# Kernel optimization log

Hardware: AMD Instinct MI355X
Metric: run time of the kernel (lower is better)

Reference implementation:

```python
import jax, jax.numpy as jnp
import numpy as np

EPS = 1e-9
SPREAD_WEIGHT = 0.1
QUAD_WEIGHT = 1.0

N_NODES = 200000
N_EDGES = 12800000
DIM = 128


def to_uhg_space(x):
    # dim > 2: truncate to first 2 features, append homogeneous 1 -> [..., 3]
    ones = jnp.ones((*x.shape[:-1], 1), dtype=x.dtype)
    return jnp.concatenate([x[..., :2], ones], axis=-1)


def uhg_inner(a, b):
    # -<spatial,spatial> + time*time, keepdim
    return -jnp.sum(a[..., :-1] * b[..., :-1], axis=-1, keepdims=True) + a[..., -1:] * b[..., -1:]


def uhg_quadrance(a, b):
    aa = uhg_inner(a, a)
    bb = uhg_inner(b, b)
    ab = uhg_inner(a, b)
    num = ab * ab - aa * bb
    den = aa * bb
    safe = jnp.maximum(jnp.abs(den), EPS) * jnp.sign(den)
    return (num / safe).squeeze(-1)


# spread has the identical formula, applied to lines instead of points
uhg_spread = uhg_quadrance


def setup_inputs() -> dict:
    key = jax.random.key(0)
    k1, k2 = jax.random.split(key)
    z = jax.random.normal(k1, (N_NODES, DIM), dtype=jnp.float32)
    edge_index = jax.random.randint(k2, (2, N_EDGES), 0, N_NODES, dtype=jnp.int32)
    return {"z": z, "edge_index": edge_index}


def reference(z, edge_index):
    z_uhg = to_uhg_space(z)                      # [N, 3]
    src, dst = edge_index[0], edge_index[1]
    # proximity: quadrance over all edges (gather + fused elementwise + mean)
    quad = uhg_quadrance(z_uhg[src], z_uhg[dst])  # [E]
    proximity_loss = quad.mean()
    # compactness: quadrance of every node to the origin [0,0,1]
    origin = jnp.zeros((1, 3), dtype=z.dtype).at[:, -1].set(1.0)
    compactness_loss = uhg_quadrance(z_uhg, origin).mean()
    # lines: vectorized cross product of each point with the origin
    lines = jnp.cross(z_uhg, origin)              # [N, 3]
    # spread over the first min(10, E) edges only (as in the original)
    n_sp = min(10, edge_index.shape[1])
    sp = uhg_spread(lines[src[:n_sp]], lines[dst[:n_sp]])
    spread_loss = sp.mean()
    loss = QUAD_WEIGHT * (proximity_loss + compactness_loss) + SPREAD_WEIGHT * spread_loss
    return loss
```

## Files before the change

kernel.cpp:

```cpp
#include <hip/hip_runtime.h>
#include <hip/hip_bf16.h>

#define UHG_EPS 1e-9
#define ZDIM 128

#define EDGE_BLOCKS 2048
#define NODE_BLOCKS 1024
#define BLOCK 256

#define PROX_OFF 0
#define COMP_OFF (16 * 1024)
#define TABLE_OFF (24 * 1024)

typedef float vfloat2 __attribute__((ext_vector_type(2)));
typedef int vint4 __attribute__((ext_vector_type(4)));

__device__ vfloat2 llvm_amdgcn_raw_buffer_load_v2f32(vint4 rsrc, int voffset, int soffset,
                                                     int cpol) __asm("llvm.amdgcn.raw.buffer.load.v2f32");

__device__ __forceinline__ vint4 make_srd(const void* base, unsigned int bytes) {
    union { const void* p; unsigned int w[2]; } pb;
    pb.p = base;
    vint4 r;
    r.x = (int)pb.w[0];
    r.y = (int)pb.w[1];
    r.z = (int)bytes;
    r.w = 0x00020000;
    return r;
}


__device__ __forceinline__ double safe_den(double den) {
    return copysign(fmax(fabs(den), UHG_EPS), den);
}

__device__ __forceinline__ double quad_xy(vfloat2 a, vfloat2 b) {
    double xa = a.x, ya = a.y, xb = b.x, yb = b.y;
    double aa = 1.0 - (xa * xa + ya * ya);
    double bb = 1.0 - (xb * xb + yb * yb);
    double ab = 1.0 - (xa * xb + ya * yb);
    double den = aa * bb;
    double num = ab * ab - den;
    return num / safe_den(den);
}

__device__ __forceinline__ double block_reduce(double v, double* sh) {
    int lane = threadIdx.x & 63;
    int wid = threadIdx.x >> 6;
    v += __shfl_down(v, 32);
    v += __shfl_down(v, 16);
    v += __shfl_down(v, 8);
    v += __shfl_down(v, 4);
    v += __shfl_down(v, 2);
    v += __shfl_down(v, 1);
    if (lane == 0) sh[wid] = v;
    __syncthreads();
    double r = 0.0;
    if (wid == 0) {
        int nw = blockDim.x >> 6;
        r = (lane < nw) ? sh[lane] : 0.0;
        r += __shfl_down(r, 4);
        r += __shfl_down(r, 2);
        r += __shfl_down(r, 1);
    }
    __syncthreads();
    return r;
}


__global__ __launch_bounds__(BLOCK) void node_kernel(const float* __restrict__ z,
                                                     vfloat2* __restrict__ table,
                                                     double* __restrict__ comp_partials, int N) {
    __shared__ double sh[8];
    const vfloat2* zp = (const vfloat2*)z;
    double local = 0.0;
    for (int i = blockIdx.x * BLOCK + threadIdx.x; i < N; i += NODE_BLOCKS * BLOCK) {
        vfloat2 v = zp[(size_t)i * (ZDIM / 2)];
        if (table) table[i] = v;
        double x = v.x, y = v.y;
        double aa = 1.0 - (x * x + y * y);
        local += (1.0 - aa) / safe_den(aa);
    }
    double tot = block_reduce(local, sh);
    if (threadIdx.x == 0) comp_partials[blockIdx.x] = tot;
}

template <int COMPACT>
__global__ __launch_bounds__(BLOCK) void edge_kernel(const vint4* __restrict__ src4,
                                                     const vint4* __restrict__ dst4, int nvec,
                                                     const int* __restrict__ src,
                                                     const int* __restrict__ dst, int E,
                                                     const void* __restrict__ xy, int N,
                                                     double* __restrict__ prox_partials) {
    __shared__ double sh[8];
    double local = 0.0;
    int tid = blockIdx.x * BLOCK + threadIdx.x;
    const int gstride = EDGE_BLOCKS * BLOCK;
    const int SHIFT = COMPACT ? 3 : 9;

    vint4 srd = make_srd(xy, COMPACT ? (unsigned int)N * 8u : (unsigned int)N * 512u);

    int nvec2 = nvec / 2;
    int v = tid;
    vint4 s0n = {}, s1n = {}, d0n = {}, d1n = {};
    if (v < nvec2) {
        s0n = __builtin_nontemporal_load(src4 + 2 * v);
        s1n = __builtin_nontemporal_load(src4 + 2 * v + 1);
        d0n = __builtin_nontemporal_load(dst4 + 2 * v);
        d1n = __builtin_nontemporal_load(dst4 + 2 * v + 1);
    }
    while (v < nvec2) {
        vint4 s0 = s0n, s1 = s1n, d0 = d0n, d1 = d1n;
        int vn = v + gstride;
        if (vn < nvec2) {
            s0n = __builtin_nontemporal_load(src4 + 2 * vn);
            s1n = __builtin_nontemporal_load(src4 + 2 * vn + 1);
            d0n = __builtin_nontemporal_load(dst4 + 2 * vn);
            d1n = __builtin_nontemporal_load(dst4 + 2 * vn + 1);
        }
        vfloat2 a0 = llvm_amdgcn_raw_buffer_load_v2f32(srd, s0.x << SHIFT, 0, 1);
        vfloat2 a1 = llvm_amdgcn_raw_buffer_load_v2f32(srd, s0.y << SHIFT, 0, 1);
        vfloat2 a2 = llvm_amdgcn_raw_buffer_load_v2f32(srd, s0.z << SHIFT, 0, 1);
        vfloat2 a3 = llvm_amdgcn_raw_buffer_load_v2f32(srd, s0.w << SHIFT, 0, 1);
        vfloat2 a4 = llvm_amdgcn_raw_buffer_load_v2f32(srd, s1.x << SHIFT, 0, 1);
        vfloat2 a5 = llvm_amdgcn_raw_buffer_load_v2f32(srd, s1.y << SHIFT, 0, 1);
        vfloat2 a6 = llvm_amdgcn_raw_buffer_load_v2f32(srd, s1.z << SHIFT, 0, 1);
        vfloat2 a7 = llvm_amdgcn_raw_buffer_load_v2f32(srd, s1.w << SHIFT, 0, 1);
        vfloat2 b0 = llvm_amdgcn_raw_buffer_load_v2f32(srd, d0.x << SHIFT, 0, 1);
        vfloat2 b1 = llvm_amdgcn_raw_buffer_load_v2f32(srd, d0.y << SHIFT, 0, 1);
        vfloat2 b2 = llvm_amdgcn_raw_buffer_load_v2f32(srd, d0.z << SHIFT, 0, 1);
        vfloat2 b3 = llvm_amdgcn_raw_buffer_load_v2f32(srd, d0.w << SHIFT, 0, 1);
        vfloat2 b4 = llvm_amdgcn_raw_buffer_load_v2f32(srd, d1.x << SHIFT, 0, 1);
        vfloat2 b5 = llvm_amdgcn_raw_buffer_load_v2f32(srd, d1.y << SHIFT, 0, 1);
        vfloat2 b6 = llvm_amdgcn_raw_buffer_load_v2f32(srd, d1.z << SHIFT, 0, 1);
        vfloat2 b7 = llvm_amdgcn_raw_buffer_load_v2f32(srd, d1.w << SHIFT, 0, 1);
        local += quad_xy(a0, b0);
        local += quad_xy(a1, b1);
        local += quad_xy(a2, b2);
        local += quad_xy(a3, b3);
        local += quad_xy(a4, b4);
        local += quad_xy(a5, b5);
        local += quad_xy(a6, b6);
        local += quad_xy(a7, b7);
        v = vn;
    }
    for (int e = 8 * nvec2 + tid; e < E; e += gstride) {
        vfloat2 a = llvm_amdgcn_raw_buffer_load_v2f32(srd, src[e] << SHIFT, 0, 1);
        vfloat2 b = llvm_amdgcn_raw_buffer_load_v2f32(srd, dst[e] << SHIFT, 0, 1);
        local += quad_xy(a, b);
    }
    double tot = block_reduce(local, sh);
    if (threadIdx.x == 0) prox_partials[blockIdx.x] = tot;
}

__global__ __launch_bounds__(BLOCK) void finalize_kernel(const int* __restrict__ src,
                                                         const int* __restrict__ dst,
                                                         const float* __restrict__ z,
                                                         const double* __restrict__ prox_partials,
                                                         const double* __restrict__ comp_partials,
                                                         float* __restrict__ out, int N, int E) {
    __shared__ double sh[8];
    int t = threadIdx.x;

    double pl = 0.0;
    for (int i = t; i < EDGE_BLOCKS; i += BLOCK) pl += prox_partials[i];
    double prox = block_reduce(pl, sh);

    double cl = 0.0;
    for (int i = t; i < NODE_BLOCKS; i += BLOCK) cl += comp_partials[i];
    double comp = block_reduce(cl, sh);

    int n_sp = E < 10 ? E : 10;
    double sl = 0.0;
    if (t < n_sp) {
        int s = src[t], d = dst[t];
        double xa = z[(size_t)s * ZDIM], ya = z[(size_t)s * ZDIM + 1];
        double xb = z[(size_t)d * ZDIM], yb = z[(size_t)d * ZDIM + 1];
        double aa = -(ya * ya + xa * xa);
        double bb = -(yb * yb + xb * xb);
        double ab = -(ya * yb + xa * xb);
        double den = aa * bb;
        sl = (ab * ab - den) / safe_den(den);
    }
    double spread = block_reduce(sl, sh);

    if (t == 0) {
        double loss = prox / (double)E + comp / (double)N;
        if (n_sp > 0) loss += 0.1 * (spread / (double)n_sp);
        out[0] = (float)loss;
    }
}


extern "C" void kernel_launch(void* const* d_in, const int* in_sizes, int n_in,
                              void* d_out, int out_size, void* d_ws, size_t ws_size,
                              hipStream_t stream) {
    const float* z = (const float*)d_in[0];
    const int* edge_index = (const int*)d_in[1];
    float* out = (float*)d_out;

    const int N = in_sizes[0] / ZDIM;
    const int E = in_sizes[1] / 2;
    const int* src = edge_index;
    const int* dst = edge_index + (size_t)E;

    double* prox_partials = (double*)((char*)d_ws + PROX_OFF);
    double* comp_partials = (double*)((char*)d_ws + COMP_OFF);
    vfloat2* table = (vfloat2*)((char*)d_ws + TABLE_OFF);
    bool use_table = ws_size >= TABLE_OFF + (size_t)N * sizeof(vfloat2);

    node_kernel<<<NODE_BLOCKS, BLOCK, 0, stream>>>(z, use_table ? table : nullptr,
                                                   comp_partials, N);

    int nvec = E / 4;
    if (use_table) {
        edge_kernel<1><<<EDGE_BLOCKS, BLOCK, 0, stream>>>((const vint4*)src, (const vint4*)dst,
                                                          nvec, src, dst, E, table, N,
                                                          prox_partials);
    } else {
        edge_kernel<0><<<EDGE_BLOCKS, BLOCK, 0, stream>>>((const vint4*)src, (const vint4*)dst,
                                                          nvec, src, dst, E, z, N,
                                                          prox_partials);
    }

    finalize_kernel<<<1, BLOCK, 0, stream>>>(src, dst, z, prox_partials, comp_partials,
                                             out, N, E);
}
```

Baseline: 294.1 us.

## Software-pipeline edge gathers two iterations deep and halve edge grid

Restructures the edge loop into a two-stage software pipeline. Each iteration issues the table gathers for the next batch of 8 edges and loads the index vectors two batches ahead, then does the quadrance math on the current batch. A sched_barrier keeps the compiler from reordering the loads past the compute. The edge grid also drops from 2048 to 1024 blocks, so each thread covers more iterations and the pipeline has more steady-state work. The cost is higher register pressure from the 32 extra in-flight float2 values, which may lower occupancy.

```diff
diff --git a/kernel.cpp b/kernel.cpp
--- a/kernel.cpp
+++ b/kernel.cpp
@@ -4,7 +4,7 @@
 #define UHG_EPS 1e-9
 #define ZDIM 128
 
-#define EDGE_BLOCKS 2048
+#define EDGE_BLOCKS 1024
 #define NODE_BLOCKS 1024
 #define BLOCK 256
 
@@ -85,6 +85,16 @@
     if (threadIdx.x == 0) comp_partials[blockIdx.x] = tot;
 }
 
+#define GATHER8(dsta, i0, i1)                                                   \
+    dsta[0] = llvm_amdgcn_raw_buffer_load_v2f32(srd, (i0).x << SHIFT, 0, 1);    \
+    dsta[1] = llvm_amdgcn_raw_buffer_load_v2f32(srd, (i0).y << SHIFT, 0, 1);    \
+    dsta[2] = llvm_amdgcn_raw_buffer_load_v2f32(srd, (i0).z << SHIFT, 0, 1);    \
+    dsta[3] = llvm_amdgcn_raw_buffer_load_v2f32(srd, (i0).w << SHIFT, 0, 1);    \
+    dsta[4] = llvm_amdgcn_raw_buffer_load_v2f32(srd, (i1).x << SHIFT, 0, 1);    \
+    dsta[5] = llvm_amdgcn_raw_buffer_load_v2f32(srd, (i1).y << SHIFT, 0, 1);    \
+    dsta[6] = llvm_amdgcn_raw_buffer_load_v2f32(srd, (i1).z << SHIFT, 0, 1);    \
+    dsta[7] = llvm_amdgcn_raw_buffer_load_v2f32(srd, (i1).w << SHIFT, 0, 1);
+
 template <int COMPACT>
 __global__ __launch_bounds__(BLOCK) void edge_kernel(const vint4* __restrict__ src4,
                                                      const vint4* __restrict__ dst4, int nvec,
@@ -101,49 +111,54 @@
     vint4 srd = make_srd(xy, COMPACT ? (unsigned int)N * 8u : (unsigned int)N * 512u);
 
     int nvec2 = nvec / 2;
-    int v = tid;
-    vint4 s0n = {}, s1n = {}, d0n = {}, d1n = {};
-    if (v < nvec2) {
-        s0n = __builtin_nontemporal_load(src4 + 2 * v);
-        s1n = __builtin_nontemporal_load(src4 + 2 * v + 1);
-        d0n = __builtin_nontemporal_load(dst4 + 2 * v);
-        d1n = __builtin_nontemporal_load(dst4 + 2 * v + 1);
-    }
-    while (v < nvec2) {
-        vint4 s0 = s0n, s1 = s1n, d0 = d0n, d1 = d1n;
-        int vn = v + gstride;
-        if (vn < nvec2) {
-            s0n = __builtin_nontemporal_load(src4 + 2 * vn);
-            s1n = __builtin_nontemporal_load(src4 + 2 * vn + 1);
-            d0n = __builtin_nontemporal_load(dst4 + 2 * vn);
-            d1n = __builtin_nontemporal_load(dst4 + 2 * vn + 1);
+
+    int v0 = tid;
+    bool p0 = v0 < nvec2;
+    int v1 = v0 + gstride;
+    bool p1 = v1 < nvec2;
+
+    vint4 is0 = {}, is1 = {}, id0 = {}, id1 = {};
+    vfloat2 ca[8] = {}, cb[8] = {};
+    vfloat2 na[8] = {}, nb[8] = {};
+
+    if (p0) {
+        vint4 s0 = __builtin_nontemporal_load(src4 + 2 * (long)v0);
+        vint4 s1 = __builtin_nontemporal_load(src4 + 2 * (long)v0 + 1);
+        vint4 d0 = __builtin_nontemporal_load(dst4 + 2 * (long)v0);
+        vint4 d1 = __builtin_nontemporal_load(dst4 + 2 * (long)v0 + 1);
+        GATHER8(ca, s0, s1);
+        GATHER8(cb, d0, d1);
+    }
+    if (p1) {
+        is0 = __builtin_nontemporal_load(src4 + 2 * (long)v1);
+        is1 = __builtin_nontemporal_load(src4 + 2 * (long)v1 + 1);
+        id0 = __builtin_nontemporal_load(dst4 + 2 * (long)v1);
+        id1 = __builtin_nontemporal_load(dst4 + 2 * (long)v1 + 1);
+    }
+
+    while (p0) {
+        if (p1) {
+            GATHER8(na, is0, is1);
+            GATHER8(nb, id0, id1);
         }
-        vfloat2 a0 = llvm_amdgcn_raw_buffer_load_v2f32(srd, s0.x << SHIFT, 0, 1);
-        vfloat2 a1 = llvm_amdgcn_raw_buffer_load_v2f32(srd, s0.y << SHIFT, 0, 1);
-        vfloat2 a2 = llvm_amdgcn_raw_buffer_load_v2f32(srd, s0.z << SHIFT, 0, 1);
-        vfloat2 a3 = llvm_amdgcn_raw_buffer_load_v2f32(srd, s0.w << SHIFT, 0, 1);
-        vfloat2 a4 = llvm_amdgcn_raw_buffer_load_v2f32(srd, s1.x << SHIFT, 0, 1);
-        vfloat2 a5 = llvm_amdgcn_raw_buffer_load_v2f32(srd, s1.y << SHIFT, 0, 1);
-        vfloat2 a6 = llvm_amdgcn_raw_buffer_load_v2f32(srd, s1.z << SHIFT, 0, 1);
-        vfloat2 a7 = llvm_amdgcn_raw_buffer_load_v2f32(srd, s1.w << SHIFT, 0, 1);
-        vfloat2 b0 = llvm_amdgcn_raw_buffer_load_v2f32(srd, d0.x << SHIFT, 0, 1);
-        vfloat2 b1 = llvm_amdgcn_raw_buffer_load_v2f32(srd, d0.y << SHIFT, 0, 1);
-        vfloat2 b2 = llvm_amdgcn_raw_buffer_load_v2f32(srd, d0.z << SHIFT, 0, 1);
-        vfloat2 b3 = llvm_amdgcn_raw_buffer_load_v2f32(srd, d0.w << SHIFT, 0, 1);
-        vfloat2 b4 = llvm_amdgcn_raw_buffer_load_v2f32(srd, d1.x << SHIFT, 0, 1);
-        vfloat2 b5 = llvm_amdgcn_raw_buffer_load_v2f32(srd, d1.y << SHIFT, 0, 1);
-        vfloat2 b6 = llvm_amdgcn_raw_buffer_load_v2f32(srd, d1.z << SHIFT, 0, 1);
-        vfloat2 b7 = llvm_amdgcn_raw_buffer_load_v2f32(srd, d1.w << SHIFT, 0, 1);
-        local += quad_xy(a0, b0);
-        local += quad_xy(a1, b1);
-        local += quad_xy(a2, b2);
-        local += quad_xy(a3, b3);
-        local += quad_xy(a4, b4);
-        local += quad_xy(a5, b5);
-        local += quad_xy(a6, b6);
-        local += quad_xy(a7, b7);
-        v = vn;
-    }
+        int v2 = v1 + gstride;
+        bool p2 = v2 < nvec2;
+        if (p2) {
+            is0 = __builtin_nontemporal_load(src4 + 2 * (long)v2);
+            is1 = __builtin_nontemporal_load(src4 + 2 * (long)v2 + 1);
+            id0 = __builtin_nontemporal_load(dst4 + 2 * (long)v2);
+            id1 = __builtin_nontemporal_load(dst4 + 2 * (long)v2 + 1);
+        }
+        __builtin_amdgcn_sched_barrier(0);
+#pragma unroll
+        for (int i = 0; i < 8; ++i) local += quad_xy(ca[i], cb[i]);
+#pragma unroll
+        for (int i = 0; i < 8; ++i) { ca[i] = na[i]; cb[i] = nb[i]; }
+        p0 = p1;
+        v1 = v2;
+        p1 = p2;
+    }
+
     for (int e = 8 * nvec2 + tid; e < E; e += gstride) {
         vfloat2 a = llvm_amdgcn_raw_buffer_load_v2f32(srd, src[e] << SHIFT, 0, 1);
         vfloat2 b = llvm_amdgcn_raw_buffer_load_v2f32(srd, dst[e] << SHIFT, 0, 1);
```

Result: no change. 292.4 us (-0.6%).
